# Optimization experiments

Measured on AMD Instinct MI355X. Metric: run time of the kernel, lower is better.

The kernel has to match this reference:

```python
import jax, jax.numpy as jnp
import numpy as np

B, S, D = 2, 2048, 1024        # batch, seq_len, d_model
E, F, K = 8, 2048, 2           # num_experts, ffn_hidden_size, moe_top_k


def setup_inputs() -> dict:
    key = jax.random.key(0)
    k0, k1, k2, k3, k4 = jax.random.split(key, 5)
    scale = 0.02
    x = jax.random.normal(k0, (B, S, D), dtype=jnp.float32)
    w1 = jax.random.normal(k1, (E * F, D), dtype=jnp.float32) * scale
    v1 = jax.random.normal(k2, (E * F, D), dtype=jnp.float32) * scale
    w2 = jax.random.normal(k3, (E * F, D), dtype=jnp.float32) * scale
    router_w = jax.random.normal(k4, (E, D), dtype=jnp.float32) * scale
    return {"x": x, "w1": w1, "v1": v1, "w2": w2, "router_w": router_w}


def reference(x, w1, v1, w2, router_w):
    # ---- Router (deterministic; no jitter) ----
    logits = jnp.einsum("bsd,ed->bse", x, router_w)              # (B,S,E)
    weights = jax.nn.softmax(logits.astype(jnp.float32), axis=-1)
    top_weights, top_experts = jax.lax.top_k(weights, K)          # (B,S,K)
    # moe_normalize_expert_weights = 1 -> L1 renormalization of top-k weights
    norm = jnp.sum(jnp.abs(top_weights), axis=-1, keepdims=True)
    top_weights = (top_weights / norm).astype(x.dtype)

    # ---- Experts: dense SwiGLU per expert, masked combine (faithful to loop) ----
    w1e = w1.reshape(E, F, D)
    v1e = v1.reshape(E, F, D)
    w2e = w2.reshape(E, F, D)
    out = jnp.zeros_like(x)
    for e in range(E):  # fixed small expert count; structurally distinct weights
        gate = jnp.sum(jnp.where(top_experts == e, top_weights, 0.0), axis=-1)  # (B,S)
        h1 = jax.nn.silu(jnp.einsum("bsd,fd->bsf", x, w1e[e]))
        h = h1 * jnp.einsum("bsd,fd->bsf", x, v1e[e])             # (B,S,F)
        y = jnp.einsum("bsf,fd->bsd", h, w2e[e])                  # (B,S,D)
        out = out + gate[..., None] * y
    return out
```

## Files before the change

### kernel.cpp

```cpp
#include <hip/hip_runtime.h>
#include <hip/hip_bf16.h>
#include <stdint.h>

#define D_MODEL 1024
#define NEXP 8
#define FF 2048
#define TOPK 2
#define NTOK 4096
#define MT 128
#define KSTEP 32
#define MAXROWS (NTOK*TOPK + NEXP*MT)
#define MAXTILES (MAXROWS/MT)

typedef __bf16 bf16x8 __attribute__((ext_vector_type(8)));
typedef float f32x4 __attribute__((ext_vector_type(4)));

__device__ inline unsigned short f2b(float f){
  __hip_bfloat16 h = __float2bfloat16(f);
  return __builtin_bit_cast(unsigned short, h);
}

__device__ inline void gl2lds16(const unsigned short* g, unsigned short* l){
  __builtin_amdgcn_global_load_lds(
      (const __attribute__((address_space(1))) unsigned int*)g,
      (__attribute__((address_space(3))) unsigned int*)l, 16, 0, 0);
}

__global__ void zero_out_kernel(float* out, int n){
  int i = blockIdx.x*256 + threadIdx.x;
  if (i < n) out[i] = 0.f;
}

__global__ __launch_bounds__(256) void conv_kernel(
    const float* __restrict__ in, unsigned short* __restrict__ out, long n4)
{
  long i = (long)blockIdx.x*256 + threadIdx.x;
  if (i >= n4) return;
  float4 v = reinterpret_cast<const float4*>(in)[i];
  ushort4 o;
  o.x = f2b(v.x); o.y = f2b(v.y); o.z = f2b(v.z); o.w = f2b(v.w);
  reinterpret_cast<ushort4*>(out)[i] = o;
}


__global__ void init_kernel(int* perm, int* ctrl){
  int i = blockIdx.x*256 + threadIdx.x;
  if (i < MAXROWS) perm[i] = -1;
  if (i < 64) ctrl[i] = 0;
}

__global__ __launch_bounds__(256) void router_kernel(
    const float* __restrict__ x, const float* __restrict__ rw,
    float* __restrict__ topw, int* __restrict__ tope, int* __restrict__ counts)
{
  const int wid = threadIdx.x >> 6, lane = threadIdx.x & 63;
  const int t = blockIdx.x*4 + wid;
  float p[NEXP];
  #pragma unroll
  for (int e=0;e<NEXP;e++) p[e] = 0.f;
  for (int i=0;i<16;i++){
    int d = i*64 + lane;
    float xv = x[(long)t*D_MODEL + d];
    #pragma unroll
    for (int e=0;e<NEXP;e++) p[e] += xv * rw[e*D_MODEL + d];
  }
  #pragma unroll
  for (int e=0;e<NEXP;e++)
    for (int off=32; off; off>>=1) p[e] += __shfl_xor(p[e], off, 64);
  if (lane == 0){
    float mx = p[0];
    #pragma unroll
    for (int e=1;e<NEXP;e++) mx = fmaxf(mx, p[e]);
    float w[NEXP]; float s = 0.f;
    #pragma unroll
    for (int e=0;e<NEXP;e++){ w[e] = expf(p[e]-mx); s += w[e]; }
    #pragma unroll
    for (int e=0;e<NEXP;e++) w[e] /= s;
    int e1 = 0;
    #pragma unroll
    for (int e=1;e<NEXP;e++) if (w[e] > w[e1]) e1 = e;
    int e2 = -1;
    #pragma unroll
    for (int e=0;e<NEXP;e++) if (e != e1 && (e2 < 0 || w[e] > w[e2])) e2 = e;
    float s2 = w[e1] + w[e2];
    topw[t*2+0] = w[e1]/s2;
    topw[t*2+1] = w[e2]/s2;
    tope[t*2+0] = e1; tope[t*2+1] = e2;
    atomicAdd(&counts[e1], 1); atomicAdd(&counts[e2], 1);
  }
}

__global__ void partition_kernel(const int* ctrl, int* segStart, int* tileExpert){
  if (threadIdx.x == 0 && blockIdx.x == 0){
    int off = 0, tile = 0;
    for (int e=0;e<NEXP;e++){
      segStart[e] = off;
      int padded = ((ctrl[e] + MT - 1)/MT)*MT;
      off += padded;
      for (int k=0;k<padded/MT && tile < MAXTILES;k++) tileExpert[tile++] = e;
    }
    segStart[NEXP] = off;
    while (tile < MAXTILES) tileExpert[tile++] = -1;
  }
}

__global__ void scatter_kernel(const int* tope, const int* segStart, int* fill,
                               int* perm, int* rowOf){
  int i = blockIdx.x*256 + threadIdx.x;
  int e = tope[i];
  int pos = segStart[e] + atomicAdd(&fill[e], 1);
  if (pos >= 0 && pos < MAXROWS){ perm[pos] = i >> 1; rowOf[i] = pos; }
}

__global__ void transpose_w2(const float* __restrict__ w2,
                             unsigned short* __restrict__ w2t){
  __shared__ unsigned short tl[32][33];
  const int e = blockIdx.z;
  const int d0 = blockIdx.x*32, f0 = blockIdx.y*32;
  const int tx = threadIdx.x, ty = threadIdx.y;
  #pragma unroll
  for (int i=0;i<4;i++)
    tl[ty + i*8][tx] = f2b(w2[((long)(e*FF + f0 + ty + i*8))*D_MODEL + d0 + tx]);
  __syncthreads();
  #pragma unroll
  for (int i=0;i<4;i++)
    w2t[((long)e*D_MODEL + d0 + ty + i*8)*FF + f0 + tx] = tl[tx][ty + i*8];
}

__global__ __launch_bounds__(256, 2) void gemm1_swiglu(
    const unsigned short* __restrict__ x,
    const unsigned short* __restrict__ w1,
    const unsigned short* __restrict__ v1,
    const int* __restrict__ perm,
    const int* __restrict__ tileExpert,
    unsigned short* __restrict__ Hg)
{
  const int b = blockIdx.x;
  const int xcd = b & 7, s = b >> 3;
  const int mt = xcd*9 + (s % 9);
  const int nt = s / 9;
  int e = tileExpert[mt];
  if (e < 0) return;
  e &= 7;
  __shared__ alignas(16) unsigned short As [2][MT*KSTEP];
  __shared__ alignas(16) unsigned short B1s[2][MT*KSTEP];
  __shared__ alignas(16) unsigned short B2s[2][MT*KSTEP];
  const int tid = threadIdx.x;
  const int lane = tid & 63;
  const int wr = ((tid >> 7) & 1) * 64;
  const int wc = ((tid >> 6) & 1) * 64;

  long aoff[2]; long boff[2]; int dstIdx[2];
  #pragma unroll
  for (int i=0;i<2;i++){
    int idx = tid + 256*i;
    int r = idx >> 2, c = idx & 3;
    int sc = c ^ ((r >> 1) & 3);
    int tok = perm[mt*MT + r]; if (tok < 0 || tok >= NTOK) tok = 0;
    aoff[i] = (long)tok * D_MODEL + sc*8;
    boff[i] = ((long)e*FF + nt*MT + r) * D_MODEL + sc*8;
    dstIdx[i] = idx * 8;
  }
  f32x4 zero = {0.f,0.f,0.f,0.f};
  f32x4 acc1[4][4], acc2[4][4];
  #pragma unroll
  for (int i=0;i<4;i++)
    #pragma unroll
    for (int j=0;j<4;j++){ acc1[i][j] = zero; acc2[i][j] = zero; }

  #pragma unroll
  for (int i=0;i<2;i++) gl2lds16(x  + aoff[i], &As [0][dstIdx[i]]);
  #pragma unroll
  for (int i=0;i<2;i++) gl2lds16(w1 + boff[i], &B1s[0][dstIdx[i]]);
  #pragma unroll
  for (int i=0;i<2;i++) gl2lds16(v1 + boff[i], &B2s[0][dstIdx[i]]);

  const int NK = D_MODEL / KSTEP;
  #pragma unroll 2
  for (int t=0; t<NK; ++t){
    const int cur = t & 1;
    if (t+1 < NK){
      const int k0 = (t+1)*KSTEP;
      #pragma unroll
      for (int i=0;i<2;i++) gl2lds16(x  + aoff[i] + k0, &As [cur^1][dstIdx[i]]);
      #pragma unroll
      for (int i=0;i<2;i++) gl2lds16(w1 + boff[i] + k0, &B1s[cur^1][dstIdx[i]]);
      #pragma unroll
      for (int i=0;i<2;i++) gl2lds16(v1 + boff[i] + k0, &B2s[cur^1][dstIdx[i]]);
      asm volatile("s_waitcnt vmcnt(6)" ::: "memory");
    } else {
      asm volatile("s_waitcnt vmcnt(0)" ::: "memory");
    }
    __builtin_amdgcn_s_barrier();
    asm volatile("" ::: "memory");

    const int q = lane >> 4;
    bf16x8 a[4], bb1[4], bb2[4];
    #pragma unroll
    for (int i=0;i<4;i++){
      int r = wr + i*16 + (lane & 15);
      a[i] = *reinterpret_cast<const bf16x8*>(&As[cur][r*KSTEP + ((q ^ ((r>>1)&3))*8)]);
    }
    #pragma unroll
    for (int j=0;j<4;j++){
      int n = wc + j*16 + (lane & 15);
      int adr = n*KSTEP + ((q ^ ((n>>1)&3))*8);
      bb1[j] = *reinterpret_cast<const bf16x8*>(&B1s[cur][adr]);
      bb2[j] = *reinterpret_cast<const bf16x8*>(&B2s[cur][adr]);
    }
    #pragma unroll
    for (int i=0;i<4;i++)
      #pragma unroll
      for (int j=0;j<4;j++){
        acc1[i][j] = __builtin_amdgcn_mfma_f32_16x16x32_bf16(a[i], bb1[j], acc1[i][j], 0,0,0);
        acc2[i][j] = __builtin_amdgcn_mfma_f32_16x16x32_bf16(a[i], bb2[j], acc2[i][j], 0,0,0);
      }
    asm volatile("s_waitcnt lgkmcnt(0)" ::: "memory");
    __builtin_amdgcn_s_barrier();
    asm volatile("" ::: "memory");
  }
  const int mrow0 = mt*MT + wr + ((lane >> 4) << 2);
  const int ncol0 = nt*MT + wc + (lane & 15);
  #pragma unroll
  for (int i=0;i<4;i++)
    #pragma unroll
    for (int j=0;j<4;j++)
      #pragma unroll
      for (int rr=0;rr<4;rr++){
        float g = acc1[i][j][rr];
        float u = acc2[i][j][rr];
        float h = (g / (1.0f + __expf(-g))) * u;
        Hg[(long)(mrow0 + i*16 + rr)*FF + (ncol0 + j*16)] = f2b(h);
      }
}

__global__ __launch_bounds__(256, 3) void gemm2_kernel(
    const unsigned short* __restrict__ Hg,
    const unsigned short* __restrict__ w2t,
    const int* __restrict__ tileExpert,
    float* __restrict__ Yg)
{
  const int b = blockIdx.x;
  const int xcd = b & 7, s = b >> 3;
  const int mt = xcd + 8*(s >> 3);
  const int nt = s & 7;
  int e = tileExpert[mt];
  if (e < 0) return;
  e &= 7;
  __shared__ alignas(16) unsigned short As[2][MT*KSTEP];
  __shared__ alignas(16) unsigned short Bs[2][MT*KSTEP];
  const int tid = threadIdx.x;
  const int lane = tid & 63;
  const int wr = ((tid >> 7) & 1) * 64;
  const int wc = ((tid >> 6) & 1) * 64;

  long aoff[2]; long boff[2]; int dstIdx[2];
  #pragma unroll
  for (int i=0;i<2;i++){
    int idx = tid + 256*i;
    int r = idx >> 2, c = idx & 3;
    int sc = c ^ ((r >> 1) & 3);
    aoff[i] = (long)(mt*MT + r) * FF + sc*8;
    boff[i] = ((long)e*D_MODEL + nt*MT + r) * FF + sc*8;
    dstIdx[i] = idx * 8;
  }
  f32x4 zero = {0.f,0.f,0.f,0.f};
  f32x4 acc[4][4];
  #pragma unroll
  for (int i=0;i<4;i++)
    #pragma unroll
    for (int j=0;j<4;j++) acc[i][j] = zero;

  #pragma unroll
  for (int i=0;i<2;i++) gl2lds16(Hg  + aoff[i], &As[0][dstIdx[i]]);
  #pragma unroll
  for (int i=0;i<2;i++) gl2lds16(w2t + boff[i], &Bs[0][dstIdx[i]]);

  const int NK = FF / KSTEP;
  #pragma unroll 2
  for (int t=0; t<NK; ++t){
    const int cur = t & 1;
    if (t+1 < NK){
      const int k0 = (t+1)*KSTEP;
      #pragma unroll
      for (int i=0;i<2;i++) gl2lds16(Hg  + aoff[i] + k0, &As[cur^1][dstIdx[i]]);
      #pragma unroll
      for (int i=0;i<2;i++) gl2lds16(w2t + boff[i] + k0, &Bs[cur^1][dstIdx[i]]);
      asm volatile("s_waitcnt vmcnt(4)" ::: "memory");
    } else {
      asm volatile("s_waitcnt vmcnt(0)" ::: "memory");
    }
    __builtin_amdgcn_s_barrier();
    asm volatile("" ::: "memory");

    const int q = lane >> 4;
    bf16x8 a[4], bb[4];
    #pragma unroll
    for (int i=0;i<4;i++){
      int r = wr + i*16 + (lane & 15);
      a[i] = *reinterpret_cast<const bf16x8*>(&As[cur][r*KSTEP + ((q ^ ((r>>1)&3))*8)]);
    }
    #pragma unroll
    for (int j=0;j<4;j++){
      int n = wc + j*16 + (lane & 15);
      bb[j] = *reinterpret_cast<const bf16x8*>(&Bs[cur][n*KSTEP + ((q ^ ((n>>1)&3))*8)]);
    }
    #pragma unroll
    for (int i=0;i<4;i++)
      #pragma unroll
      for (int j=0;j<4;j++)
        acc[i][j] = __builtin_amdgcn_mfma_f32_16x16x32_bf16(a[i], bb[j], acc[i][j], 0,0,0);

    asm volatile("s_waitcnt lgkmcnt(0)" ::: "memory");
    __builtin_amdgcn_s_barrier();
    asm volatile("" ::: "memory");
  }
  const int mrow0 = mt*MT + wr + ((lane >> 4) << 2);
  const int ncol0 = nt*MT + wc + (lane & 15);
  #pragma unroll
  for (int i=0;i<4;i++)
    #pragma unroll
    for (int j=0;j<4;j++)
      #pragma unroll
      for (int rr=0;rr<4;rr++)
        Yg[(long)(mrow0 + i*16 + rr)*D_MODEL + (ncol0 + j*16)] = acc[i][j][rr];
}

__global__ __launch_bounds__(256) void combine_kernel(
    const float* __restrict__ Yg, const float* __restrict__ topw,
    const int* __restrict__ rowOf, float* __restrict__ out)
{
  const int t = blockIdx.x;
  const int d = threadIdx.x * 4;
  const float wA = topw[2*t], wB = topw[2*t+1];
  long rA = rowOf[2*t], rB = rowOf[2*t+1];
  if (rA < 0 || rA >= MAXROWS) rA = 0;
  if (rB < 0 || rB >= MAXROWS) rB = 0;
  float4 a = *reinterpret_cast<const float4*>(Yg + rA*D_MODEL + d);
  float4 b = *reinterpret_cast<const float4*>(Yg + rB*D_MODEL + d);
  float4 o;
  o.x = wA*a.x + wB*b.x;
  o.y = wA*a.y + wB*b.y;
  o.z = wA*a.z + wB*b.z;
  o.w = wA*a.w + wB*b.w;
  *reinterpret_cast<float4*>(out + (long)t*D_MODEL + d) = o;
}

extern "C" void kernel_launch(void* const* d_in, const int* in_sizes, int n_in,
                              void* d_out, int out_size, void* d_ws, size_t ws_size,
                              hipStream_t stream)
{
  const float* x  = (const float*)d_in[0];
  const float* w1 = (const float*)d_in[1];
  const float* v1 = (const float*)d_in[2];
  const float* w2 = (const float*)d_in[3];
  const float* rw = (const float*)d_in[4];
  float* out = (float*)d_out;
  (void)in_sizes; (void)n_in;

  size_t need = 0;
  auto count = [&](size_t b){ size_t r = need; need += (b + 255) & ~(size_t)255; return r; };
  size_t o_topw = count((size_t)NTOK*TOPK*sizeof(float));
  size_t o_tope = count((size_t)NTOK*TOPK*sizeof(int));
  size_t o_ctrl = count(64*sizeof(int));
  size_t o_seg  = count(16*sizeof(int));
  size_t o_te   = count(MAXTILES*sizeof(int));
  size_t o_perm = count(MAXROWS*sizeof(int));
  size_t o_rowOf= count((size_t)NTOK*TOPK*sizeof(int));
  size_t o_xb   = count((size_t)NTOK*D_MODEL*2);
  size_t o_w1b  = count((size_t)NEXP*FF*D_MODEL*2);
  size_t o_v1b  = count((size_t)NEXP*FF*D_MODEL*2);
  size_t o_w2t  = count((size_t)NEXP*D_MODEL*FF*2);
  size_t o_Hg   = count((size_t)MAXROWS*FF*2);
  size_t o_Yg   = count((size_t)MAXROWS*D_MODEL*sizeof(float));

  if (ws_size < need){
    zero_out_kernel<<<(out_size+255)/256, 256, 0, stream>>>(out, out_size);
    return;
  }

  char* base = (char*)d_ws;
  float* topw      = (float*)(base + o_topw);
  int*   tope      = (int*)  (base + o_tope);
  int*   ctrl      = (int*)  (base + o_ctrl);
  int*   segStart  = (int*)  (base + o_seg);
  int*   tileExpert= (int*)  (base + o_te);
  int*   perm      = (int*)  (base + o_perm);
  int*   rowOf     = (int*)  (base + o_rowOf);
  unsigned short* xb  = (unsigned short*)(base + o_xb);
  unsigned short* w1b = (unsigned short*)(base + o_w1b);
  unsigned short* v1b = (unsigned short*)(base + o_v1b);
  unsigned short* w2t = (unsigned short*)(base + o_w2t);
  unsigned short* Hg  = (unsigned short*)(base + o_Hg);
  float*          Yg  = (float*)         (base + o_Yg);

  const long nx4 = (long)NTOK*D_MODEL/4;
  const long nw4 = (long)NEXP*FF*D_MODEL/4;

  init_kernel     <<<(MAXROWS+255)/256, 256, 0, stream>>>(perm, ctrl);
  router_kernel   <<<NTOK/4, 256, 0, stream>>>(x, rw, topw, tope, ctrl);
  partition_kernel<<<1, 64, 0, stream>>>(ctrl, segStart, tileExpert);
  scatter_kernel  <<<NTOK*TOPK/256, 256, 0, stream>>>(tope, segStart, ctrl+8, perm, rowOf);
  conv_kernel     <<<(nx4+255)/256, 256, 0, stream>>>(x,  xb,  nx4);
  conv_kernel     <<<(nw4+255)/256, 256, 0, stream>>>(w1, w1b, nw4);
  conv_kernel     <<<(nw4+255)/256, 256, 0, stream>>>(v1, v1b, nw4);
  transpose_w2    <<<dim3(D_MODEL/32, FF/32, NEXP), dim3(32,8), 0, stream>>>(w2, w2t);
  gemm1_swiglu    <<<MAXTILES*(FF/MT), 256, 0, stream>>>(xb, w1b, v1b, perm, tileExpert, Hg);
  gemm2_kernel    <<<MAXTILES*(D_MODEL/MT), 256, 0, stream>>>(Hg, w2t, tileExpert, Yg);
  combine_kernel  <<<NTOK, 256, 0, stream>>>(Yg, topw, rowOf, out);
}
```

Baseline: 534.8 us.

## Triple-buffer LDS in both MoE GEMMs and fuse x bf16 conversion into router

```diff
diff --git a/kernel.cpp b/kernel.cpp
--- a/kernel.cpp
+++ b/kernel.cpp
@@ -51,18 +51,25 @@
 
 __global__ __launch_bounds__(256) void router_kernel(
     const float* __restrict__ x, const float* __restrict__ rw,
-    float* __restrict__ topw, int* __restrict__ tope, int* __restrict__ counts)
+    float* __restrict__ topw, int* __restrict__ tope, int* __restrict__ counts,
+    unsigned short* __restrict__ xb)
 {
   const int wid = threadIdx.x >> 6, lane = threadIdx.x & 63;
   const int t = blockIdx.x*4 + wid;
   float p[NEXP];
   #pragma unroll
   for (int e=0;e<NEXP;e++) p[e] = 0.f;
-  for (int i=0;i<16;i++){
-    int d = i*64 + lane;
-    float xv = x[(long)t*D_MODEL + d];
-    #pragma unroll
-    for (int e=0;e<NEXP;e++) p[e] += xv * rw[e*D_MODEL + d];
+  #pragma unroll
+  for (int j=0;j<4;j++){
+    const int d4 = j*64 + lane;
+    float4 xv = reinterpret_cast<const float4*>(x + (long)t*D_MODEL)[d4];
+    ushort4 o; o.x=f2b(xv.x); o.y=f2b(xv.y); o.z=f2b(xv.z); o.w=f2b(xv.w);
+    reinterpret_cast<ushort4*>(xb + (long)t*D_MODEL)[d4] = o;
+    #pragma unroll
+    for (int e=0;e<NEXP;e++){
+      float4 rv = reinterpret_cast<const float4*>(rw + e*D_MODEL)[d4];
+      p[e] += xv.x*rv.x + xv.y*rv.y + xv.z*rv.z + xv.w*rv.w;
+    }
   }
   #pragma unroll
   for (int e=0;e<NEXP;e++)
@@ -142,13 +149,17 @@
   int e = tileExpert[mt];
   if (e < 0) return;
   e &= 7;
-  __shared__ alignas(16) unsigned short As [2][MT*KSTEP];
-  __shared__ alignas(16) unsigned short B1s[2][MT*KSTEP];
-  __shared__ alignas(16) unsigned short B2s[2][MT*KSTEP];
+  __shared__ alignas(16) unsigned short As [3][MT*KSTEP];
+  __shared__ alignas(16) unsigned short B1s[3][MT*KSTEP];
+  __shared__ alignas(16) unsigned short B2s[3][MT*KSTEP];
   const int tid = threadIdx.x;
   const int lane = tid & 63;
   const int wr = ((tid >> 7) & 1) * 64;
   const int wc = ((tid >> 6) & 1) * 64;
+  unsigned short* const As0  = &As [0][0];
+  unsigned short* const B1s0 = &B1s[0][0];
+  unsigned short* const B2s0 = &B2s[0][0];
+  const int BSZ = MT*KSTEP;
 
   long aoff[2]; long boff[2]; int dstIdx[2];
   #pragma unroll
@@ -169,24 +180,33 @@
     for (int j=0;j<4;j++){ acc1[i][j] = zero; acc2[i][j] = zero; }
 
   #pragma unroll
-  for (int i=0;i<2;i++) gl2lds16(x  + aoff[i], &As [0][dstIdx[i]]);
-  #pragma unroll
-  for (int i=0;i<2;i++) gl2lds16(w1 + boff[i], &B1s[0][dstIdx[i]]);
-  #pragma unroll
-  for (int i=0;i<2;i++) gl2lds16(v1 + boff[i], &B2s[0][dstIdx[i]]);
+  for (int i=0;i<2;i++) gl2lds16(x  + aoff[i],          As0  + dstIdx[i]);
+  #pragma unroll
+  for (int i=0;i<2;i++) gl2lds16(w1 + boff[i],          B1s0 + dstIdx[i]);
+  #pragma unroll
+  for (int i=0;i<2;i++) gl2lds16(v1 + boff[i],          B2s0 + dstIdx[i]);
+  #pragma unroll
+  for (int i=0;i<2;i++) gl2lds16(x  + aoff[i] + KSTEP,  As0  + BSZ + dstIdx[i]);
+  #pragma unroll
+  for (int i=0;i<2;i++) gl2lds16(w1 + boff[i] + KSTEP,  B1s0 + BSZ + dstIdx[i]);
+  #pragma unroll
+  for (int i=0;i<2;i++) gl2lds16(v1 + boff[i] + KSTEP,  B2s0 + BSZ + dstIdx[i]);
 
   const int NK = D_MODEL / KSTEP;
-  #pragma unroll 2
+  int cur = 0;
   for (int t=0; t<NK; ++t){
-    const int cur = t & 1;
-    if (t+1 < NK){
-      const int k0 = (t+1)*KSTEP;
-      #pragma unroll
-      for (int i=0;i<2;i++) gl2lds16(x  + aoff[i] + k0, &As [cur^1][dstIdx[i]]);
-      #pragma unroll
-      for (int i=0;i<2;i++) gl2lds16(w1 + boff[i] + k0, &B1s[cur^1][dstIdx[i]]);
-      #pragma unroll
-      for (int i=0;i<2;i++) gl2lds16(v1 + boff[i] + k0, &B2s[cur^1][dstIdx[i]]);
+    if (t+2 < NK){
+      const int pf = (cur == 0) ? 2 : cur-1;
+      const long k0 = (long)(t+2)*KSTEP;
+      const int pdst = pf*BSZ;
+      #pragma unroll
+      for (int i=0;i<2;i++) gl2lds16(x  + aoff[i] + k0, As0  + pdst + dstIdx[i]);
+      #pragma unroll
+      for (int i=0;i<2;i++) gl2lds16(w1 + boff[i] + k0, B1s0 + pdst + dstIdx[i]);
+      #pragma unroll
+      for (int i=0;i<2;i++) gl2lds16(v1 + boff[i] + k0, B2s0 + pdst + dstIdx[i]);
+      asm volatile("s_waitcnt vmcnt(12)" ::: "memory");
+    } else if (t+1 < NK){
       asm volatile("s_waitcnt vmcnt(6)" ::: "memory");
     } else {
       asm volatile("s_waitcnt vmcnt(0)" ::: "memory");
@@ -194,19 +214,22 @@
     __builtin_amdgcn_s_barrier();
     asm volatile("" ::: "memory");
 
+    const unsigned short* Ac  = As0  + cur*BSZ;
+    const unsigned short* B1c = B1s0 + cur*BSZ;
+    const unsigned short* B2c = B2s0 + cur*BSZ;
     const int q = lane >> 4;
     bf16x8 a[4], bb1[4], bb2[4];
     #pragma unroll
     for (int i=0;i<4;i++){
       int r = wr + i*16 + (lane & 15);
-      a[i] = *reinterpret_cast<const bf16x8*>(&As[cur][r*KSTEP + ((q ^ ((r>>1)&3))*8)]);
+      a[i] = *reinterpret_cast<const bf16x8*>(&Ac[r*KSTEP + ((q ^ ((r>>1)&3))*8)]);
     }
     #pragma unroll
     for (int j=0;j<4;j++){
       int n = wc + j*16 + (lane & 15);
       int adr = n*KSTEP + ((q ^ ((n>>1)&3))*8);
-      bb1[j] = *reinterpret_cast<const bf16x8*>(&B1s[cur][adr]);
-      bb2[j] = *reinterpret_cast<const bf16x8*>(&B2s[cur][adr]);
+      bb1[j] = *reinterpret_cast<const bf16x8*>(&B1c[adr]);
+      bb2[j] = *reinterpret_cast<const bf16x8*>(&B2c[adr]);
     }
     #pragma unroll
     for (int i=0;i<4;i++)
@@ -218,6 +241,7 @@
     asm volatile("s_waitcnt lgkmcnt(0)" ::: "memory");
     __builtin_amdgcn_s_barrier();
     asm volatile("" ::: "memory");
+    cur = (cur == 2) ? 0 : cur+1;
   }
   const int mrow0 = mt*MT + wr + ((lane >> 4) << 2);
   const int ncol0 = nt*MT + wc + (lane & 15);
@@ -247,12 +271,15 @@
   int e = tileExpert[mt];
   if (e < 0) return;
   e &= 7;
-  __shared__ alignas(16) unsigned short As[2][MT*KSTEP];
-  __shared__ alignas(16) unsigned short Bs[2][MT*KSTEP];
+  __shared__ alignas(16) unsigned short As[3][MT*KSTEP];
+  __shared__ alignas(16) unsigned short Bs[3][MT*KSTEP];
   const int tid = threadIdx.x;
   const int lane = tid & 63;
   const int wr = ((tid >> 7) & 1) * 64;
   const int wc = ((tid >> 6) & 1) * 64;
+  unsigned short* const As0 = &As[0][0];
+  unsigned short* const Bs0 = &Bs[0][0];
+  const int BSZ = MT*KSTEP;
 
   long aoff[2]; long boff[2]; int dstIdx[2];
   #pragma unroll
@@ -272,20 +299,27 @@
     for (int j=0;j<4;j++) acc[i][j] = zero;
 
   #pragma unroll
-  for (int i=0;i<2;i++) gl2lds16(Hg  + aoff[i], &As[0][dstIdx[i]]);
-  #pragma unroll
-  for (int i=0;i<2;i++) gl2lds16(w2t + boff[i], &Bs[0][dstIdx[i]]);
+  for (int i=0;i<2;i++) gl2lds16(Hg  + aoff[i],          As0 + dstIdx[i]);
+  #pragma unroll
+  for (int i=0;i<2;i++) gl2lds16(w2t + boff[i],          Bs0 + dstIdx[i]);
+  #pragma unroll
+  for (int i=0;i<2;i++) gl2lds16(Hg  + aoff[i] + KSTEP,  As0 + BSZ + dstIdx[i]);
+  #pragma unroll
+  for (int i=0;i<2;i++) gl2lds16(w2t + boff[i] + KSTEP,  Bs0 + BSZ + dstIdx[i]);
 
   const int NK = FF / KSTEP;
-  #pragma unroll 2
+  int cur = 0;
   for (int t=0; t<NK; ++t){
-    const int cur = t & 1;
-    if (t+1 < NK){
-      const int k0 = (t+1)*KSTEP;
-      #pragma unroll
-      for (int i=0;i<2;i++) gl2lds16(Hg  + aoff[i] + k0, &As[cur^1][dstIdx[i]]);
-      #pragma unroll
-      for (int i=0;i<2;i++) gl2lds16(w2t + boff[i] + k0, &Bs[cur^1][dstIdx[i]]);
+    if (t+2 < NK){
+      const int pf = (cur == 0) ? 2 : cur-1;
+      const long k0 = (long)(t+2)*KSTEP;
+      const int pdst = pf*BSZ;
+      #pragma unroll
+      for (int i=0;i<2;i++) gl2lds16(Hg  + aoff[i] + k0, As0 + pdst + dstIdx[i]);
+      #pragma unroll
+      for (int i=0;i<2;i++) gl2lds16(w2t + boff[i] + k0, Bs0 + pdst + dstIdx[i]);
+      asm volatile("s_waitcnt vmcnt(8)" ::: "memory");
+    } else if (t+1 < NK){
       asm volatile("s_waitcnt vmcnt(4)" ::: "memory");
     } else {
       asm volatile("s_waitcnt vmcnt(0)" ::: "memory");
@@ -293,17 +327,19 @@
     __builtin_amdgcn_s_barrier();
     asm volatile("" ::: "memory");
 
+    const unsigned short* Ac = As0 + cur*BSZ;
+    const unsigned short* Bc = Bs0 + cur*BSZ;
     const int q = lane >> 4;
     bf16x8 a[4], bb[4];
     #pragma unroll
     for (int i=0;i<4;i++){
       int r = wr + i*16 + (lane & 15);
-      a[i] = *reinterpret_cast<const bf16x8*>(&As[cur][r*KSTEP + ((q ^ ((r>>1)&3))*8)]);
+      a[i] = *reinterpret_cast<const bf16x8*>(&Ac[r*KSTEP + ((q ^ ((r>>1)&3))*8)]);
     }
     #pragma unroll
     for (int j=0;j<4;j++){
       int n = wc + j*16 + (lane & 15);
-      bb[j] = *reinterpret_cast<const bf16x8*>(&Bs[cur][n*KSTEP + ((q ^ ((n>>1)&3))*8)]);
+      bb[j] = *reinterpret_cast<const bf16x8*>(&Bc[n*KSTEP + ((q ^ ((n>>1)&3))*8)]);
     }
     #pragma unroll
     for (int i=0;i<4;i++)
@@ -314,6 +350,7 @@
     asm volatile("s_waitcnt lgkmcnt(0)" ::: "memory");
     __builtin_amdgcn_s_barrier();
     asm volatile("" ::: "memory");
+    cur = (cur == 2) ? 0 : cur+1;
   }
   const int mrow0 = mt*MT + wr + ((lane >> 4) << 2);
   const int ncol0 = nt*MT + wc + (lane & 15);
@@ -394,14 +431,12 @@
   unsigned short* Hg  = (unsigned short*)(base + o_Hg);
   float*          Yg  = (float*)         (base + o_Yg);
 
-  const long nx4 = (long)NTOK*D_MODEL/4;
   const long nw4 = (long)NEXP*FF*D_MODEL/4;
 
   init_kernel     <<<(MAXROWS+255)/256, 256, 0, stream>>>(perm, ctrl);
-  router_kernel   <<<NTOK/4, 256, 0, stream>>>(x, rw, topw, tope, ctrl);
+  router_kernel   <<<NTOK/4, 256, 0, stream>>>(x, rw, topw, tope, ctrl, xb);
   partition_kernel<<<1, 64, 0, stream>>>(ctrl, segStart, tileExpert);
   scatter_kernel  <<<NTOK*TOPK/256, 256, 0, stream>>>(tope, segStart, ctrl+8, perm, rowOf);
-  conv_kernel     <<<(nx4+255)/256, 256, 0, stream>>>(x,  xb,  nx4);
   conv_kernel     <<<(nw4+255)/256, 256, 0, stream>>>(w1, w1b, nw4);
   conv_kernel     <<<(nw4+255)/256, 256, 0, stream>>>(v1, v1b, nw4);
   transpose_w2    <<<dim3(D_MODEL/32, FF/32, NEXP), dim3(32,8), 0, stream>>>(w2, w2t);
```

New measurement: 538.7 us. Within noise of the previous version (+0.7%).
